# Kernel optimization log

Measured on AMD Instinct MI355X. Metric: run time of the kernel, lower is better.

Reference implementation:

```python
import jax, jax.numpy as jnp
import numpy as np

B_GRAPHS = 16      # number of graphs in batch
NPG = 8192         # nodes per graph
N = B_GRAPHS * NPG # 131072 total nodes
F_DIM = 64         # node feature dim
K_CLUST = 16       # n_clusters
DEG = 32           # avg degree
E = N * DEG        # 4,194,304 edges


def setup_inputs() -> dict:
    key = jax.random.key(0)
    k1, k2, k3, k4, k5 = jax.random.split(key, 5)
    x = jax.random.normal(k1, (N, F_DIM), jnp.float32)
    W = jax.random.normal(k2, (F_DIM, K_CLUST), jnp.float32) / np.sqrt(F_DIM)
    b = jnp.zeros((K_CLUST,), jnp.float32)
    # edges constrained within each graph -> block-diagonal adjacency (PyG batching)
    g = jnp.repeat(jnp.arange(B_GRAPHS, dtype=jnp.int32), E // B_GRAPHS)
    edge_row = g * NPG + jax.random.randint(k3, (E,), 0, NPG, jnp.int32)
    edge_col = g * NPG + jax.random.randint(k4, (E,), 0, NPG, jnp.int32)
    edge_weight = jax.random.uniform(k5, (E,), jnp.float32)
    return {"x": x, "W": W, "b": b, "edge_weight": edge_weight,
            "edge_row": edge_row, "edge_col": edge_col, "num_graphs": B_GRAPHS}


def _forward(x, W, b, edge_weight, edge_row, edge_col, num_graphs):
    Ntot, Fd = x.shape
    K = W.shape[1]
    Bn = num_graphs
    n = Ntot // Bn  # equal-size graphs (ptr = n * arange(B+1))

    s = x @ W + b                                   # [N,K] cluster logits
    xb = x.reshape(Bn, n, Fd)
    sb = s.reshape(Bn, n, K)
    # out_x = selu(s^T @ x_bd), block b = s_b^T x_b, then hsplit_and_vstack -> [B*K, F]
    out_x = jax.nn.selu(jnp.einsum('bnk,bnf->bkf', sb, xb)).reshape(Bn * K, Fd)

    ss = jax.nn.softmax(s, axis=-1)                 # softmaxed assignments
    ssb = ss.reshape(Bn, n, K)

    # degree d = adj.sum(axis=0)  (column sums over COO edges)
    d = jax.ops.segment_sum(edge_weight, edge_col, num_segments=Ntot)   # [N]
    m2 = d.reshape(Bn, n).sum(1)                    # total degree per graph [B]

    # A @ C via edge scatter: (A C)[row] += w * C[col]
    AC = jax.ops.segment_sum(edge_weight[:, None] * ss[edge_col], edge_row,
                             num_segments=Ntot)     # [N,K]
    # out_adj blocks: C_b^T A_b C_b  -> [B,K,K]
    out_adj = jnp.einsum('bnk,bnl->bkl', ssb, AC.reshape(Bn, n, K))

    # dS_b = C_b^T d_b  (Ca/Cb blocks); normalizer gets m_inv twice in torch code
    dS = jnp.einsum('bn,bnk->bk', d.reshape(Bn, n), ssb)                # [B,K]
    spectral_loss = -jnp.mean(jnp.einsum('bkk->b', out_adj) / m2
                              - (dS ** 2).sum(1) / (m2 ** 2))

    sqrt_K = jnp.sqrt(jnp.float32(K))
    cluster_size = ssb.sum(1)                        # [B,K]
    cluster_loss = jnp.mean(jnp.sqrt((cluster_size ** 2).sum(1)) / n * sqrt_K - 1.0)

    # CC blocks: C_b^T C_b; ortho = mean_b || CC_b/||CC_b||_F - I/sqrt(K) ||_F
    CC = jnp.einsum('bnk,bnl->bkl', ssb, ssb)        # [B,K,K]
    CC_norm = jnp.sqrt((CC ** 2).sum((1, 2)))        # Frobenius norm per block
    eye_div_k = jnp.eye(K, dtype=x.dtype) / sqrt_K
    ortho_loss = jnp.mean(jnp.sqrt(
        ((CC / CC_norm[:, None, None] - eye_div_k) ** 2).sum((1, 2))))

    # mask diagonal and degree-normalize pooled adjacency
    oa = out_adj * (1.0 - jnp.eye(K, dtype=x.dtype))
    dd = jnp.sqrt(oa.sum(2)) + 1e-12                 # row sums per block [B,K]
    out_adj_norm = oa / (dd[:, :, None] * dd[:, None, :])

    return out_x, out_adj_norm, spectral_loss, cluster_loss, ortho_loss


def reference(x, W, b, edge_weight, edge_row, edge_col, num_graphs):
    return _forward(x, W, b, edge_weight, edge_row, edge_col, num_graphs)
```

## Files before the change

kernel.cpp:

```cpp
#include <hip/hip_runtime.h>
#include <math.h>

#define F_DIM 64
#define K_CL 16
#define B_GR 16
#define SROW 72

typedef _Float16 h16;
using f16x8 = __attribute__((ext_vector_type(8))) _Float16;
using f32x4 = __attribute__((ext_vector_type(4))) float;

__global__ __launch_bounds__(256) void k_fused(
    const float* __restrict__ x, const float* __restrict__ W, const float* __restrict__ bvec,
    h16* __restrict__ ssh, float* __restrict__ outx, float* __restrict__ CCb)
{
    __shared__ float Wl[F_DIM * K_CL];
    __shared__ float bl[K_CL];
    __shared__ __align__(16) h16 stage[4][(16 + 16 + 64) * SROW];

    int t = threadIdx.x;
    for (int idx = t; idx < F_DIM * K_CL; idx += 256) Wl[idx] = W[idx];
    if (t < K_CL) bl[t] = bvec[t];
    __syncthreads();

    int wid = t >> 6, lane = t & 63;
    h16* Sg = stage[wid];
    h16* Cg = Sg + 16 * SROW;
    h16* Xg = Cg + 16 * SROW;

    size_t i = (size_t)blockIdx.x * 256 + t;
    float s[16];
#pragma unroll
    for (int k = 0; k < 16; ++k) s[k] = bl[k];

    const float4* xp = reinterpret_cast<const float4*>(x + i * F_DIM);
#pragma unroll
    for (int j = 0; j < 16; ++j) {
        float4 q = xp[j];
        float xf[4] = {q.x, q.y, q.z, q.w};
#pragma unroll
        for (int ff = 0; ff < 4; ++ff) {
            int f = j * 4 + ff;
            float xv = xf[ff];
            Xg[f * SROW + lane] = (h16)xv;
            const float4* wr = reinterpret_cast<const float4*>(&Wl[f * K_CL]);
            float4 w0 = wr[0], w1 = wr[1], w2 = wr[2], w3 = wr[3];
            s[0]  += xv * w0.x; s[1]  += xv * w0.y; s[2]  += xv * w0.z; s[3]  += xv * w0.w;
            s[4]  += xv * w1.x; s[5]  += xv * w1.y; s[6]  += xv * w1.z; s[7]  += xv * w1.w;
            s[8]  += xv * w2.x; s[9]  += xv * w2.y; s[10] += xv * w2.z; s[11] += xv * w2.w;
            s[12] += xv * w3.x; s[13] += xv * w3.y; s[14] += xv * w3.z; s[15] += xv * w3.w;
        }
    }

#pragma unroll
    for (int k = 0; k < 16; ++k) Sg[k * SROW + lane] = (h16)s[k];

    float m = s[0];
#pragma unroll
    for (int k = 1; k < 16; ++k) m = fmaxf(m, s[k]);
    float sum = 0.f;
#pragma unroll
    for (int k = 0; k < 16; ++k) { s[k] = __expf(s[k] - m); sum += s[k]; }
    float inv = 1.0f / sum;
#pragma unroll
    for (int k = 0; k < 16; ++k) s[k] *= inv;

    f16x8 h0, h1;
#pragma unroll
    for (int k = 0; k < 8; ++k) { h0[k] = (h16)s[k]; h1[k] = (h16)s[k + 8]; }
#pragma unroll
    for (int k = 0; k < 8; ++k) {
        Cg[k * SROW + lane] = h0[k];
        Cg[(k + 8) * SROW + lane] = h1[k];
    }
    f16x8* hp = reinterpret_cast<f16x8*>(ssh + i * K_CL);
    hp[0] = h0;
    hp[1] = h1;

    int q4 = lane >> 4, mm = lane & 15;
    f32x4 accO[4] = {{0.f,0.f,0.f,0.f},{0.f,0.f,0.f,0.f},{0.f,0.f,0.f,0.f},{0.f,0.f,0.f,0.f}};
    f32x4 accC = {0.f, 0.f, 0.f, 0.f};
#pragma unroll
    for (int h = 0; h < 2; ++h) {
        f16x8 aO = *(const f16x8*)&Sg[mm * SROW + h * 32 + q4 * 8];
        f16x8 aC = *(const f16x8*)&Cg[mm * SROW + h * 32 + q4 * 8];
        accC = __builtin_amdgcn_mfma_f32_16x16x32_f16(aC, aC, accC, 0, 0, 0);
#pragma unroll
        for (int ft = 0; ft < 4; ++ft) {
            f16x8 bO = *(const f16x8*)&Xg[(ft * 16 + mm) * SROW + h * 32 + q4 * 8];
            accO[ft] = __builtin_amdgcn_mfma_f32_16x16x32_f16(aO, bO, accO[ft], 0, 0, 0);
        }
    }
    __syncthreads();

    float* redO = (float*)&stage[0][0];
    float* redC = redO + 4096;
#pragma unroll
    for (int ft = 0; ft < 4; ++ft)
#pragma unroll
        for (int rg = 0; rg < 4; ++rg)
            redO[wid * 1024 + (q4 * 4 + rg) * 64 + ft * 16 + mm] = accO[ft][rg];
#pragma unroll
    for (int rg = 0; rg < 4; ++rg)
        redC[wid * 256 + (q4 * 4 + rg) * 16 + mm] = accC[rg];
    __syncthreads();

    int g = blockIdx.x >> 5;
#pragma unroll
    for (int it = 0; it < 4; ++it) {
        int idx = t + it * 256;
        float v = redO[idx] + redO[1024 + idx] + redO[2048 + idx] + redO[3072 + idx];
        atomicAdd(outx + g * 1024 + idx, v);
    }
    {
        float v = redC[t] + redC[256 + t] + redC[512 + t] + redC[768 + t];
        atomicAdd(CCb + g * 256 + t, v);
    }
}

__global__ __launch_bounds__(256) void k_edge(
    const int* __restrict__ erow, const int* __restrict__ ecol, const float* __restrict__ ew,
    const h16* __restrict__ ssh, float* __restrict__ oadj,
    int edges_per_block, int edges_per_graph, int nmask)
{
    __shared__ float CCl[256];
    __shared__ __align__(16) h16 stageE[4][32 * SROW];
    int t = threadIdx.x;
    CCl[t] = 0.f;
    __syncthreads();

    int bid = blockIdx.x;
    int xcd = bid & 7;
    int slot = bid >> 3;
    int graph = xcd + 8 * (slot & 1);
    int chunk = slot >> 1;

    int wid = t >> 6, lane = t & 63;
    int q4 = lane >> 4, mm = lane & 15;
    h16* Ag = stageE[wid];
    h16* Bg = Ag + 16 * SROW;

    int epw = edges_per_block >> 2;
    size_t base = (size_t)graph * edges_per_graph
                + (size_t)chunk * edges_per_block
                + (size_t)wid * epw;

    const f16x8* sshp = reinterpret_cast<const f16x8*>(ssh);
    f32x4 acc = {0.f, 0.f, 0.f, 0.f};

    for (int e0 = 0; e0 < epw; e0 += 64) {
        size_t eb = base + e0 + lane;
        int   r = erow[eb] & nmask;
        int   c = ecol[eb] & nmask;
        float w = ew[eb];

        f16x8 a0 = sshp[2 * (size_t)r];
        f16x8 a1 = sshp[2 * (size_t)r + 1];
        f16x8 b0 = sshp[2 * (size_t)c];
        f16x8 b1 = sshp[2 * (size_t)c + 1];
        h16 wh = (h16)w;
#pragma unroll
        for (int k = 0; k < 8; ++k) { a0[k] *= wh; a1[k] *= wh; }

#pragma unroll
        for (int k = 0; k < 8; ++k) {
            Ag[k * SROW + lane]       = a0[k];
            Ag[(k + 8) * SROW + lane] = a1[k];
            Bg[k * SROW + lane]       = b0[k];
            Bg[(k + 8) * SROW + lane] = b1[k];
        }

#pragma unroll
        for (int h = 0; h < 2; ++h) {
            f16x8 af = *(const f16x8*)&Ag[mm * SROW + h * 32 + q4 * 8];
            f16x8 bf = *(const f16x8*)&Bg[mm * SROW + h * 32 + q4 * 8];
            acc = __builtin_amdgcn_mfma_f32_16x16x32_f16(af, bf, acc, 0, 0, 0);
        }
    }

#pragma unroll
    for (int rg = 0; rg < 4; ++rg)
        atomicAdd(&CCl[(q4 * 4 + rg) * 16 + mm], acc[rg]);
    __syncthreads();
    atomicAdd(oadj + graph * 256 + t, CCl[t]);
}

__global__ __launch_bounds__(256) void k_final(
    const float* __restrict__ outx, const float* __restrict__ oadj,
    const float* __restrict__ CCb, float* __restrict__ out, int npg)
{
    int t = threadIdx.x;
    int gid = blockIdx.x * 256 + t;
    {
        float v = outx[gid];
        float r = (v > 0.f) ? (1.0507009873554805f * v)
                            : (1.0507009873554805f * 1.6732632423543772f * (__expf(v) - 1.0f));
        out[gid] = r;
    }

    if (blockIdx.x != 0) return;

    int b = t >> 4, k = t & 15;
    const float* oar = oadj + b * 256 + k * 16;
    const float* ccr = CCb + b * 256 + k * 16;

    float rowsum_off = 0.f, trace_c = 0.f, rowsum_all = 0.f, fro2 = 0.f, colsum = 0.f;
    float csv = 0.f;
#pragma unroll
    for (int l = 0; l < 16; ++l) {
        float v = oar[l];
        rowsum_all += v;
        if (l == k) trace_c = v; else rowsum_off += v;
        float c = ccr[l];
        fro2 += c * c;
        csv += c;
        colsum += oadj[b * 256 + l * 16 + k];
    }
    float dd = sqrtf(rowsum_off) + 1e-12f;
    __shared__ float ddl[B_GR * K_CL];
    ddl[t] = dd;

    float ds2 = colsum * colsum, cs2 = csv * csv;
    float tr = trace_c, m2 = rowsum_all;
#pragma unroll
    for (int msk = 8; msk >= 1; msk >>= 1) {
        tr   += __shfl_xor(tr,   msk, 16);
        ds2  += __shfl_xor(ds2,  msk, 16);
        cs2  += __shfl_xor(cs2,  msk, 16);
        fro2 += __shfl_xor(fro2, msk, 16);
        m2   += __shfl_xor(m2,   msk, 16);
    }
    float invfro = 1.0f / sqrtf(fro2);
    float osum = 0.f;
#pragma unroll
    for (int l = 0; l < 16; ++l) {
        float v = ccr[l] * invfro - ((l == k) ? 0.25f : 0.f);
        osum += v * v;
    }
#pragma unroll
    for (int msk = 8; msk >= 1; msk >>= 1) osum += __shfl_xor(osum, msk, 16);

    __shared__ float sp_s[B_GR], cl_s[B_GR], or_s[B_GR];
    if (k == 0) {
        sp_s[b] = tr / m2 - ds2 / (m2 * m2);
        cl_s[b] = sqrtf(cs2) / (float)npg * 4.0f - 1.0f;
        or_s[b] = sqrtf(osum);
    }
    __syncthreads();
    if (t == 0) {
        float a = 0.f, c = 0.f, o = 0.f;
        for (int i = 0; i < B_GR; ++i) { a += sp_s[i]; c += cl_s[i]; o += or_s[i]; }
        out[20480] = -a / 16.f;
        out[20481] = c / 16.f;
        out[20482] = o / 16.f;
    }

#pragma unroll
    for (int l = 0; l < 16; ++l) {
        float v = (l == k) ? 0.f : oar[l] / (dd * ddl[b * 16 + l]);
        out[16384 + b * 256 + k * 16 + l] = v;
    }
}

extern "C" void kernel_launch(void* const* d_in, const int* in_sizes, int n_in,
                              void* d_out, int out_size, void* d_ws, size_t ws_size,
                              hipStream_t stream)
{
    const float* x    = (const float*)d_in[0];
    const float* W    = (const float*)d_in[1];
    const float* bvec = (const float*)d_in[2];
    const float* ew   = (const float*)d_in[3];
    const int* erow   = (const int*)d_in[4];
    const int* ecol   = (const int*)d_in[5];

    int Ntot = in_sizes[0] / F_DIM;
    size_t E = (size_t)in_sizes[3];
    int npg  = Ntot / B_GR;
    int edges_per_graph = (int)(E / B_GR);
    int nmask = Ntot - 1;

    const int ADJ_BLOCKS = 2048;
    int edges_per_block = (int)(E / ADJ_BLOCKS);

    char* ws = (char*)d_ws;
    size_t o = 0;
    h16*   ssh   = (h16*)(ws + o);   o += (size_t)Ntot * 16 * 2;
    size_t zoff = o;
    float* outx  = (float*)(ws + o); o += (size_t)B_GR * 1024 * 4;
    float* oadj  = (float*)(ws + o); o += (size_t)B_GR * 256 * 4;
    float* CCb   = (float*)(ws + o); o += (size_t)B_GR * 256 * 4;

    hipMemsetAsync(ws + zoff, 0, o - zoff, stream);

    k_fused<<<Ntot / 256, 256, 0, stream>>>(x, W, bvec, ssh, outx, CCb);
    k_edge<<<ADJ_BLOCKS, 256, 0, stream>>>(erow, ecol, ew, ssh, oadj,
                                           edges_per_block, edges_per_graph, nmask);
    k_final<<<64, 256, 0, stream>>>(outx, oadj, CCb, (float*)d_out, npg);
}
```

Measured before the change: 175.1 us.

## Software-pipeline edge gathers and use LDS transpose reads for MFMA operands

Measured after the change: 168.1 us. 4.0% less time.

```diff
diff --git a/kernel.cpp b/kernel.cpp
--- a/kernel.cpp
+++ b/kernel.cpp
@@ -7,6 +7,7 @@
 #define SROW 72
 
 typedef _Float16 h16;
+using f16x4 = __attribute__((ext_vector_type(4))) _Float16;
 using f16x8 = __attribute__((ext_vector_type(8))) _Float16;
 using f32x4 = __attribute__((ext_vector_type(4))) float;
 
@@ -124,7 +125,7 @@
     int edges_per_block, int edges_per_graph, int nmask)
 {
     __shared__ float CCl[256];
-    __shared__ __align__(16) h16 stageE[4][32 * SROW];
+    __shared__ __align__(16) h16 stageE[4][2048];
     int t = threadIdx.x;
     CCl[t] = 0.f;
     __syncthreads();
@@ -138,9 +139,9 @@
     int wid = t >> 6, lane = t & 63;
     int q4 = lane >> 4, mm = lane & 15;
     h16* Ag = stageE[wid];
-    h16* Bg = Ag + 16 * SROW;
 
     int epw = edges_per_block >> 2;
+    int nt  = epw >> 6;
     size_t base = (size_t)graph * edges_per_graph
                 + (size_t)chunk * edges_per_block
                 + (size_t)wid * epw;
@@ -148,35 +149,74 @@
     const f16x8* sshp = reinterpret_cast<const f16x8*>(ssh);
     f32x4 acc = {0.f, 0.f, 0.f, 0.f};
 
-    for (int e0 = 0; e0 < epw; e0 += 64) {
-        size_t eb = base + e0 + lane;
-        int   r = erow[eb] & nmask;
-        int   c = ecol[eb] & nmask;
-        float w = ew[eb];
-
-        f16x8 a0 = sshp[2 * (size_t)r];
-        f16x8 a1 = sshp[2 * (size_t)r + 1];
-        f16x8 b0 = sshp[2 * (size_t)c];
-        f16x8 b1 = sshp[2 * (size_t)c + 1];
-        h16 wh = (h16)w;
+    f16x8* Aw = reinterpret_cast<f16x8*>(Ag);
+    using lds_h16 = __attribute__((address_space(3))) h16;
+    unsigned trA = (unsigned)(uintptr_t)(lds_h16*)Ag + (unsigned)(q4 * 256 + mm * 2);
+
+    auto compute_tile = [&](f16x8 a0, f16x8 a1, f16x8 b0, f16x8 b1, float wv) {
+        h16 wh = (h16)wv;
 #pragma unroll
         for (int k = 0; k < 8; ++k) { a0[k] *= wh; a1[k] *= wh; }
-
-#pragma unroll
-        for (int k = 0; k < 8; ++k) {
-            Ag[k * SROW + lane]       = a0[k];
-            Ag[(k + 8) * SROW + lane] = a1[k];
-            Bg[k * SROW + lane]       = b0[k];
-            Bg[(k + 8) * SROW + lane] = b1[k];
-        }
-
-#pragma unroll
-        for (int h = 0; h < 2; ++h) {
-            f16x8 af = *(const f16x8*)&Ag[mm * SROW + h * 32 + q4 * 8];
-            f16x8 bf = *(const f16x8*)&Bg[mm * SROW + h * 32 + q4 * 8];
-            acc = __builtin_amdgcn_mfma_f32_16x16x32_f16(af, bf, acc, 0, 0, 0);
-        }
-    }
+        Aw[lane * 2]       = a0;
+        Aw[lane * 2 + 1]   = a1;
+        Aw[128 + lane * 2]     = b0;
+        Aw[128 + lane * 2 + 1] = b1;
+
+        f16x4 xa0, xa1, xa2, xa3, xb0, xb1, xb2, xb3;
+        asm volatile(
+            "ds_read_b64_tr_b16 %0, %8\n\t"
+            "ds_read_b64_tr_b16 %1, %8 offset:128\n\t"
+            "ds_read_b64_tr_b16 %2, %8 offset:2048\n\t"
+            "ds_read_b64_tr_b16 %3, %8 offset:2176\n\t"
+            "ds_read_b64_tr_b16 %4, %8 offset:1024\n\t"
+            "ds_read_b64_tr_b16 %5, %8 offset:1152\n\t"
+            "ds_read_b64_tr_b16 %6, %8 offset:3072\n\t"
+            "ds_read_b64_tr_b16 %7, %8 offset:3200\n\t"
+            "s_waitcnt lgkmcnt(0)"
+            : "=&v"(xa0), "=&v"(xa1), "=&v"(xb0), "=&v"(xb1),
+              "=&v"(xa2), "=&v"(xa3), "=&v"(xb2), "=&v"(xb3)
+            : "v"(trA)
+            : "memory");
+        __builtin_amdgcn_sched_barrier(0);
+
+        f16x8 afL = __builtin_shufflevector(xa0, xa1, 0, 1, 2, 3, 4, 5, 6, 7);
+        f16x8 bfL = __builtin_shufflevector(xb0, xb1, 0, 1, 2, 3, 4, 5, 6, 7);
+        f16x8 afH = __builtin_shufflevector(xa2, xa3, 0, 1, 2, 3, 4, 5, 6, 7);
+        f16x8 bfH = __builtin_shufflevector(xb2, xb3, 0, 1, 2, 3, 4, 5, 6, 7);
+        acc = __builtin_amdgcn_mfma_f32_16x16x32_f16(afL, bfL, acc, 0, 0, 0);
+        acc = __builtin_amdgcn_mfma_f32_16x16x32_f16(afH, bfH, acc, 0, 0, 0);
+    };
+
+    int rC, cC; float wC;
+    {
+        size_t e = base + lane;
+        rC = erow[e]; cC = ecol[e]; wC = ew[e];
+    }
+    size_t ri = 2 * (size_t)(rC & nmask), ci = 2 * (size_t)(cC & nmask);
+    f16x8 ca0 = sshp[ri], ca1 = sshp[ri + 1];
+    f16x8 cb0 = sshp[ci], cb1 = sshp[ci + 1];
+    int rN = 0, cN = 0; float wN = 0.f;
+    if (nt > 1) {
+        size_t e = base + 64 + lane;
+        rN = erow[e]; cN = ecol[e]; wN = ew[e];
+    }
+
+    for (int tt = 0; tt < nt - 1; ++tt) {
+        size_t rj = 2 * (size_t)(rN & nmask), cj = 2 * (size_t)(cN & nmask);
+        f16x8 na0 = sshp[rj], na1 = sshp[rj + 1];
+        f16x8 nb0 = sshp[cj], nb1 = sshp[cj + 1];
+        int t2 = (tt + 2 < nt) ? (tt + 2) : 0;
+        size_t e2 = base + (size_t)t2 * 64 + lane;
+        int r2 = erow[e2], c2 = ecol[e2];
+        float w2 = ew[e2];
+
+        compute_tile(ca0, ca1, cb0, cb1, wC);
+
+        ca0 = na0; ca1 = na1; cb0 = nb0; cb1 = nb1;
+        wC = wN;
+        rN = r2; cN = c2; wN = w2;
+    }
+    compute_tile(ca0, ca1, cb0, cb1, wC);
 
 #pragma unroll
     for (int rg = 0; rg < 4; ++rg)
```
